# Kernel tuning notes

Hardware: AMD Instinct MI355X
Metric: run time of the kernel (lower is better)

Reference implementation:

```python
import jax, jax.numpy as jnp
import numpy as np

T, N, C, RADIUS = 64, 16, 256, 64
D_OUT = 2 * RADIUS + 1
TAU = 2.0
DECAY = float(np.exp(-1.0 / TAU))  # first-order leaky (LIF) filter decay
WEIGHT0 = 6.53543197272069


def setup_inputs() -> dict:
    key = jax.random.key(0)
    k1, k2 = jax.random.split(key)
    inp = jax.random.uniform(k1, (T, N, C, 2), dtype=jnp.float32)
    delay_param = jnp.arange(-RADIUS, RADIUS + 1, dtype=jnp.float32)[:, None]  # (D_out, 1)
    weight = jnp.asarray(WEIGHT0, dtype=jnp.float32)
    u = jax.random.uniform(k2, (N, C, D_OUT, 2), dtype=jnp.float32)  # bernoulli uniforms
    return {"input": inp, "delay_param": delay_param, "weight": weight, "u": u}


def reference(input, delay_param, weight, u):
    Tn, Nn, Cn, _ = input.shape
    # delay = relu(cat([_delay, -_delay], dim=1))  -> (D_out, 2), nonnegative
    delay = jax.nn.relu(jnp.concatenate([delay_param, -delay_param], axis=1))
    Do = delay.shape[0]
    # input.unsqueeze(-2).repeat(..., D_out, 1) -> (T, N, C, D_out, 2)
    x = jnp.broadcast_to(input[:, :, :, None, :], (Tn, Nn, Cn, Do, 2))
    # stochastic rounding of per-synapse delay
    bd = jnp.broadcast_to(delay[None, None], (Nn, Cn, Do, 2))
    df = jnp.floor(bd)
    rounded = jnp.where(u < bd - df, df + 1.0, df)
    # clamp so the (one-hot) spike at argmax(t) stays inside the window
    spike_t = jnp.argmax(x, axis=0)  # (N, C, D_out, 2)
    rounded = jnp.minimum(rounded, (Tn - 1 - spike_t).astype(rounded.dtype))
    d = rounded.astype(jnp.int32)
    # circular shift along time: out[t] = x[(t - d) % T]
    t_idx = jnp.arange(Tn)[:, None, None, None, None]
    idx = (t_idx - d[None]) % Tn
    shifted = jnp.take_along_axis(x, idx, axis=0)  # (T, N, C, D_out, 2)
    # LIF filter (leaky integrator over time, state reset at t=0)
    def step(v, xt):
        v = v * DECAY + xt
        return v, v
    _, filt = jax.lax.scan(step, jnp.zeros_like(shifted[0]), shifted)
    # scale by fixed synaptic weight and sum over the 2 input channels
    return jnp.sum(filt * weight, axis=-1)  # (T, N, C, D_out)
```

## Files before the change

### kernel.cpp

```cpp
#include <hip/hip_runtime.h>

#define T_DIM 64
#define NP 4096
#define D_OUTC 129
#define ROW_STRIDE (NP * D_OUTC)

__global__ __launch_bounds__(128, 8) void jeffress_kernel(
    const float* __restrict__ input,
    const float* __restrict__ delay_param,
    const float* __restrict__ weight,
    const float* __restrict__ u,
    float* __restrict__ out)
{
    __shared__ float x_lds[2][128];
    __shared__ int caps[2];

    const int p    = ((blockIdx.x & 7) << 9) | (blockIdx.x >> 3);
    const int tid  = threadIdx.x;
    const int lane = tid & 63, wave = tid >> 6;
    const float DECAY = 0.6065306597126334f;

    {
        float xv = input[(lane * NP + p) * 2 + wave];
        x_lds[wave][lane]      = xv;
        x_lds[wave][lane + 64] = xv;
        unsigned b = __float_as_uint(xv);
        b ^= (b & 0x80000000u) ? 0xffffffffu : 0x80000000u;
        unsigned long long key = ((unsigned long long)b << 32) | (unsigned)(63 - lane);
        #pragma unroll
        for (int mm = 1; mm < 64; mm <<= 1) {
            unsigned long long o = __shfl_xor(key, mm, 64);
            if (o > key) key = o;
        }
        if (lane == 0) caps[wave] = (int)(key & 0xffffffffull);
    }
    __syncthreads();

    const float w   = weight[0];
    const float c0f = (float)caps[0], c1f = (float)caps[1];

    const int d     = (wave << 6) | lane;
    const bool dual = (tid == 127);

    auto calc = [&](int dd, int& s0, int& s1) {
        float dp = delay_param[dd];
        float b0 = fmaxf(dp, 0.0f), b1 = fmaxf(-dp, 0.0f);
        float2 uu = ((const float2*)u)[p * D_OUTC + dd];
        float f0 = floorf(b0), f1 = floorf(b1);
        float r0 = (uu.x < b0 - f0) ? f0 + 1.0f : f0;
        float r1 = (uu.y < b1 - f1) ? f1 + 1.0f : f1;
        s0 = (int)fminf(r0, c0f);
        s1 = (int)fminf(r1, c1f);
    };

    int s0, s1;
    calc(d, s0, s1);
    int e0 = 0, e1 = 0;
    if (dual) calc(128, e0, e1);

    const float* x0 = &x_lds[0][64 - s0];
    const float* x1 = &x_lds[1][64 - s1];
    const float* y0 = &x_lds[0][64 - e0];
    const float* y1 = &x_lds[1][64 - e1];

    float v0 = 0.0f, v1 = 0.0f, ve0 = 0.0f, ve1 = 0.0f;
    float* rp = out + (size_t)p * D_OUTC + d;

    #pragma unroll 4
    for (int t = 0; t < T_DIM; ++t) {
        v0 = v0 * DECAY + x0[t];
        v1 = v1 * DECAY + x1[t];
        rp[0] = w * (v0 + v1);
        if (dual) {
            ve0 = ve0 * DECAY + y0[t];
            ve1 = ve1 * DECAY + y1[t];
            rp[1] = w * (ve0 + ve1);
        }
        rp += ROW_STRIDE;
    }
}

extern "C" void kernel_launch(void* const* d_in, const int* in_sizes, int n_in,
                              void* d_out, int out_size, void* d_ws, size_t ws_size,
                              hipStream_t stream) {
    const float* input       = (const float*)d_in[0];
    const float* delay_param = (const float*)d_in[1];
    const float* weight      = (const float*)d_in[2];
    const float* u           = (const float*)d_in[3];
    float* out = (float*)d_out;

    jeffress_kernel<<<NP, 128, 0, stream>>>(input, delay_param, weight, u, out);
}
```

Baseline: 163.2 us.

## Replace per-delay LIF recurrence with shared prefix-scan and closed-form correction

```diff
diff --git a/kernel.cpp b/kernel.cpp
--- a/kernel.cpp
+++ b/kernel.cpp
@@ -12,18 +12,18 @@
     const float* __restrict__ u,
     float* __restrict__ out)
 {
-    __shared__ float x_lds[2][128];
+    __shared__ float Hw0[128], Hw1[128];
     __shared__ int caps[2];
 
     const int p    = ((blockIdx.x & 7) << 9) | (blockIdx.x >> 3);
     const int tid  = threadIdx.x;
-    const int lane = tid & 63, wave = tid >> 6;
+    const int lane = tid & 63, wv = tid >> 6;
     const float DECAY = 0.6065306597126334f;
 
+    float2 xp = ((const float2*)input)[lane * NP + p];
+
     {
-        float xv = input[(lane * NP + p) * 2 + wave];
-        x_lds[wave][lane]      = xv;
-        x_lds[wave][lane + 64] = xv;
+        float xv = wv ? xp.y : xp.x;
         unsigned b = __float_as_uint(xv);
         b ^= (b & 0x80000000u) ? 0xffffffffu : 0x80000000u;
         unsigned long long key = ((unsigned long long)b << 32) | (unsigned)(63 - lane);
@@ -32,15 +32,37 @@
             unsigned long long o = __shfl_xor(key, mm, 64);
             if (o > key) key = o;
         }
-        if (lane == 0) caps[wave] = (int)(key & 0xffffffffull);
+        if (lane == 0) caps[wv] = (int)(key & 0xffffffffull);
+    }
+
+    const float w = weight[0];
+    if (wv == 0) {
+        float v0 = xp.x, v1 = xp.y;
+        const float dks[6] = {0.6065306597126334f,
+                              0.36787944117144233f,
+                              0.1353352832366127f,
+                              0.01831563888873418f,
+                              3.3546262790251185e-4f,
+                              1.1253517471925912e-7f};
+        #pragma unroll
+        for (int k = 0; k < 6; ++k) {
+            int o = 1 << k;
+            float p0 = __shfl_up(v0, o, 64);
+            float p1 = __shfl_up(v1, o, 64);
+            if (lane >= o) { v0 += dks[k] * p0; v1 += dks[k] * p1; }
+        }
+        Hw0[lane] = w * v0;
+        Hw1[lane] = w * v1;
+    }
+    __syncthreads();
+    if (wv == 1) {
+        float f = exp2f(-0.7213475204444817f * (float)(lane + 1));
+        Hw0[64 + lane] = Hw0[lane] + f * Hw0[63];
+        Hw1[64 + lane] = Hw1[lane] + f * Hw1[63];
     }
     __syncthreads();
 
-    const float w   = weight[0];
     const float c0f = (float)caps[0], c1f = (float)caps[1];
-
-    const int d     = (wave << 6) | lane;
-    const bool dual = (tid == 127);
 
     auto calc = [&](int dd, int& s0, int& s1) {
         float dp = delay_param[dd];
@@ -53,30 +75,38 @@
         s1 = (int)fminf(r1, c1f);
     };
 
-    int s0, s1;
-    calc(d, s0, s1);
-    int e0 = 0, e1 = 0;
-    if (dual) calc(128, e0, e1);
+    int s0, s1; calc(tid, s0, s1);
+    const float* pA0 = &Hw0[64 - s0];
+    const float* pA1 = &Hw1[64 - s1];
+    const float Cw = pA0[-1] + pA1[-1];
 
-    const float* x0 = &x_lds[0][64 - s0];
-    const float* x1 = &x_lds[1][64 - s1];
-    const float* y0 = &x_lds[0][64 - e0];
-    const float* y1 = &x_lds[1][64 - e1];
+    const bool dual = (tid == 127);
+    int e0 = 0, e1 = 0; if (dual) calc(128, e0, e1);
+    const float* pB0 = &Hw0[64 - e0];
+    const float* pB1 = &Hw1[64 - e1];
+    const float CwE = dual ? (pB0[-1] + pB1[-1]) : 0.0f;
 
-    float v0 = 0.0f, v1 = 0.0f, ve0 = 0.0f, ve1 = 0.0f;
-    float* rp = out + (size_t)p * D_OUTC + d;
+    float* rp = out + (size_t)p * D_OUTC + tid;
+    float Dg = DECAY;
+    const float K[8] = {1.0f, 0.6065306597126334f, 0.36787944117144233f,
+                        0.22313016014842982f, 0.1353352832366127f,
+                        0.0820849986238988f, 0.049787068367863944f,
+                        0.030197383422318501f};
 
-    #pragma unroll 4
-    for (int t = 0; t < T_DIM; ++t) {
-        v0 = v0 * DECAY + x0[t];
-        v1 = v1 * DECAY + x1[t];
-        rp[0] = w * (v0 + v1);
-        if (dual) {
-            ve0 = ve0 * DECAY + y0[t];
-            ve1 = ve1 * DECAY + y1[t];
-            rp[1] = w * (ve0 + ve1);
+    for (int tg = 0; tg < T_DIM; tg += 8) {
+        float CwD  = Cw  * Dg;
+        float CwDE = CwE * Dg;
+        #pragma unroll
+        for (int j = 0; j < 8; ++j) {
+            float val = pA0[tg + j] + pA1[tg + j] - K[j] * CwD;
+            rp[0] = val;
+            if (dual) {
+                float ve = pB0[tg + j] + pB1[tg + j] - K[j] * CwDE;
+                rp[1] = ve;
+            }
+            rp += ROW_STRIDE;
         }
-        rp += ROW_STRIDE;
+        Dg *= 0.01831563888873418f;
     }
 }
 
```

Result: no change. 162.7 us (-0.3%).
